# Kernel tuning notes

Measured on AMD Instinct MI355X. Metric: run time of the kernel, lower is better.

Reference implementation:

```python
import jax, jax.numpy as jnp
import numpy as np

B, T, H, NH = 2, 2048, 2048, 16
HD = H // NH  # 128


def setup_inputs() -> dict:
    key = jax.random.key(0)
    ks = jax.random.split(key, 7)
    s = 1.0 / np.sqrt(H)
    return {
        "x": jax.random.normal(ks[0], (B, T, H), jnp.float32),
        "cos": jax.random.uniform(ks[1], (1, 1, T, HD), jnp.float32),
        "sin": jax.random.uniform(ks[2], (1, 1, T, HD), jnp.float32),
        "Wq": jax.random.normal(ks[3], (H, H), jnp.float32) * s,
        "Wk": jax.random.normal(ks[4], (H, H), jnp.float32) * s,
        "Wv": jax.random.normal(ks[5], (H, H), jnp.float32) * s,
        "Wo": jax.random.normal(ks[6], (H, H), jnp.float32) * s,
    }


def rotate_half(x):
    d = x.shape[-1] // 2
    return jnp.concatenate([-x[..., d:], x[..., :d]], axis=-1)


def reference(x, cos, sin, Wq, Wk, Wv, Wo):
    b, t, h = x.shape
    # torch Linear: y = x @ W.T; reshape to (B, NH, T, HD)
    def proj(W):
        return jnp.einsum('bth,oh->bto', x, W).reshape(b, t, NH, HD).transpose(0, 2, 1, 3)
    q, k, v = proj(Wq), proj(Wk), proj(Wv)
    q = q * cos + rotate_half(q) * sin
    k = k * cos + rotate_half(k) * sin
    scale = 1.0 / jnp.sqrt(jnp.asarray(HD, x.dtype))
    scores = jnp.einsum('bhqd,bhkd->bhqk', q, k) * scale  # [B,NH,T,T]
    causal = jnp.tril(jnp.ones((t, t), bool))
    scores = jnp.where(causal, scores, jnp.asarray(-jnp.inf, scores.dtype))
    attn = jax.nn.softmax(scores, axis=-1)
    out = jnp.einsum('bhqk,bhkd->bhqd', attn, v)  # [B,NH,T,HD]
    out = out.transpose(0, 2, 1, 3).reshape(b, t, h)
    return jnp.einsum('bth,oh->bto', out, Wo)
```

## Files before the change

### kernel.cpp

```cpp
#include <hip/hip_runtime.h>
#include <hip/hip_bf16.h>

#define B_  2
#define T_  2048
#define H_  2048
#define NH_ 16
#define HD_ 128
#define QKVN 6144

typedef __attribute__((ext_vector_type(8))) short  short8;
typedef __attribute__((ext_vector_type(4))) float  floatx4;

__device__ __forceinline__ unsigned short f2bf(float x) {
    union { float f; unsigned int u; } c; c.f = x;
    unsigned int r = c.u + 0x7FFF + ((c.u >> 16) & 1);
    return (unsigned short)(r >> 16);
}
__device__ __forceinline__ float bf2f(unsigned short u) {
    union { float f; unsigned int i; } c;
    c.i = ((unsigned int)u) << 16;
    return c.f;
}

__device__ __forceinline__ void gload_lds16(const void* g, void* l) {
    __builtin_amdgcn_global_load_lds(
        (__attribute__((address_space(1))) void*)g,
        (__attribute__((address_space(3))) void*)l, 16, 0, 0);
}

__global__ __launch_bounds__(256) void f32_to_bf16(
    const float* __restrict__ src, unsigned short* __restrict__ dst, int n)
{
    const int i = (blockIdx.x * 256 + threadIdx.x) * 4;
    if (i < n) {
        float4 v = *(const float4*)(src + i);
        ushort4 o;
        o.x = f2bf(v.x); o.y = f2bf(v.y); o.z = f2bf(v.z); o.w = f2bf(v.w);
        *(ushort4*)(dst + i) = o;
    }
}

#define BAR()   asm volatile("s_barrier" ::: "memory")
#define SBAR()  __builtin_amdgcn_sched_barrier(0)
#define LGKM0() do { asm volatile("s_waitcnt lgkmcnt(0)" ::: "memory"); SBAR(); } while (0)
#define VM0()   asm volatile("s_waitcnt vmcnt(0)" ::: "memory")

template<int MI, int BASE>
__device__ __forceinline__ void ldAf(short8 (&d)[MI/2][2], const unsigned short* src,
                                     int wm, int n16, int quad)
{
    #pragma unroll
    for (int mi = 0; mi < MI/2; ++mi)
        #pragma unroll
        for (int ks = 0; ks < 2; ++ks)
            d[mi][ks] = *(const short8*)(src + (wm*(MI*16) + (BASE+mi)*16 + n16) * 64
                                             + (((ks*4 + quad) ^ (n16 & 7)) * 8));
}
template<int NI, int BASE>
__device__ __forceinline__ void ldBf(short8 (&d)[NI/2][2], const unsigned short* src,
                                     int wn, int n16, int quad)
{
    #pragma unroll
    for (int ni = 0; ni < NI/2; ++ni)
        #pragma unroll
        for (int ks = 0; ks < 2; ++ks)
            d[ni][ks] = *(const short8*)(src + (wn*(NI*16) + (BASE+ni)*16 + n16) * 64
                                             + (((ks*4 + quad) ^ (n16 & 7)) * 8));
}
template<int MI, int NI, int MB, int NB>
__device__ __forceinline__ void mq(floatx4 (&acc)[MI][NI],
                                   const short8 (&a)[MI/2][2],
                                   const short8 (&b)[NI/2][2])
{
    #pragma unroll
    for (int ks = 0; ks < 2; ++ks)
        #pragma unroll
        for (int mi = 0; mi < MI/2; ++mi)
            #pragma unroll
            for (int ni = 0; ni < NI/2; ++ni)
                acc[MB+mi][NB+ni] = __builtin_amdgcn_mfma_f32_16x16x32_bf16(
                    a[mi][ks], b[ni][ks], acc[MB+mi][NB+ni], 0, 0, 0);
}

template<int MI, int NI>
__device__ __forceinline__ void gt_tile(
    const unsigned short* Ac, const unsigned short* Bc,
    unsigned short* An, unsigned short* Bn,
    const unsigned short* Ap, const unsigned short* Bp,
    size_t knext, bool pre, int tid, int K,
    int wm, int wn, int n16, int quad,
    floatx4 (&acc)[MI][NI])
{
    constexpr int MH = MI/2, NH = NI/2;
    constexpr int AG = (MI*32)/64;
    constexpr int BG = (NI*64)/64;

    short8 aL[MH][2], aH[MH][2], bL[NH][2], bH[NH][2];

    ldAf<MI, 0>(aL, Ac, wm, n16, quad);
    ldBf<NI, 0>(bL, Bc, wn, n16, quad);
    if (pre) {
        #pragma unroll
        for (int h = 0; h < AG; ++h)
            gload_lds16(Ap + knext + (size_t)h * 64 * K, An + h * 4096 + (size_t)tid * 8);
    }
    BAR();
    LGKM0();
    __builtin_amdgcn_s_setprio(1);
    mq<MI, NI, 0, 0>(acc, aL, bL);
    __builtin_amdgcn_s_setprio(0);
    BAR();

    ldBf<NI, NH>(bH, Bc, wn, n16, quad);
    if (pre) {
        #pragma unroll
        for (int h = 0; h < BG; ++h)
            gload_lds16(Bp + knext + (size_t)h * 64 * K, Bn + h * 4096 + (size_t)tid * 8);
    }
    BAR();
    LGKM0();
    __builtin_amdgcn_s_setprio(1);
    mq<MI, NI, 0, NH>(acc, aL, bH);
    __builtin_amdgcn_s_setprio(0);
    BAR();

    ldAf<MI, MH>(aH, Ac, wm, n16, quad);
    BAR();
    LGKM0();
    __builtin_amdgcn_s_setprio(1);
    mq<MI, NI, MH, 0>(acc, aH, bL);
    __builtin_amdgcn_s_setprio(0);
    BAR();

    VM0();
    BAR();
    SBAR();
    __builtin_amdgcn_s_setprio(1);
    mq<MI, NI, MH, NH>(acc, aH, bH);
    __builtin_amdgcn_s_setprio(0);
    BAR();
}

template<int MI, int NI, bool BF16_OUT>
__global__ __launch_bounds__(512, 1) void gemm_t(
    const unsigned short* __restrict__ A,
    const unsigned short* __restrict__ W,
    float* __restrict__ Yf, unsigned short* __restrict__ Yb,
    int M, int N, int K)
{
    constexpr int BM = MI*32, BN = NI*64;
    constexpr int AG = BM/64, BG = BN/64;
    __shared__ __attribute__((aligned(16))) unsigned short As[2][BM * 64];
    __shared__ __attribute__((aligned(16))) unsigned short Bs[2][BN * 64];

    const int tid  = threadIdx.x;
    const int lane = tid & 63;
    const int n16  = lane & 15;
    const int quad = lane >> 4;
    const int w    = tid >> 6;
    const int wm   = w >> 2;
    const int wn   = w & 3;

    const int m0 = blockIdx.y * BM;
    const int n0 = blockIdx.x * BN;

    const int r0  = tid >> 3;
    const int g0  = ((tid & 7) ^ (r0 & 7)) * 8;
    const unsigned short* Ap = A + (size_t)(m0 + r0) * K + g0;
    const unsigned short* Bp = W + (size_t)(n0 + r0) * K + g0;

    floatx4 acc[MI][NI];
    #pragma unroll
    for (int i = 0; i < MI; i++)
        #pragma unroll
        for (int j = 0; j < NI; j++) acc[i][j] = (floatx4){0.f, 0.f, 0.f, 0.f};

    const int nt = K >> 6;

    #pragma unroll
    for (int h = 0; h < AG; ++h)
        gload_lds16(Ap + (size_t)h * 64 * K, &As[0][h * 4096 + (size_t)tid * 8]);
    #pragma unroll
    for (int h = 0; h < BG; ++h)
        gload_lds16(Bp + (size_t)h * 64 * K, &Bs[0][h * 4096 + (size_t)tid * 8]);
    VM0();
    BAR();

    for (int t = 0; t < nt; t += 2) {
        gt_tile<MI, NI>(&As[0][0], &Bs[0][0], &As[1][0], &Bs[1][0],
                        Ap, Bp, (size_t)(t + 1) << 6, (t + 1) < nt,
                        tid, K, wm, wn, n16, quad, acc);
        gt_tile<MI, NI>(&As[1][0], &Bs[1][0], &As[0][0], &Bs[0][0],
                        Ap, Bp, (size_t)(t + 2) << 6, (t + 2) < nt,
                        tid, K, wm, wn, n16, quad, acc);
    }

    #pragma unroll
    for (int mi = 0; mi < MI; ++mi) {
        const size_t rb = (size_t)(m0 + wm*(MI*16) + mi*16 + quad*4);
        #pragma unroll
        for (int r = 0; r < 4; ++r) {
            const size_t row = rb + r;
            #pragma unroll
            for (int ni = 0; ni < NI; ++ni) {
                const size_t col = n0 + wn*(NI*16) + ni*16 + n16;
                if (BF16_OUT) Yb[row * N + col] = f2bf(acc[mi][ni][r]);
                else          Yf[row * N + col] = acc[mi][ni][r];
            }
        }
    }
}

__global__ __launch_bounds__(256) void rope_convert_qk(
    const unsigned short* __restrict__ qkvp,
    const float* __restrict__ cosp, const float* __restrict__ sinp,
    unsigned short* __restrict__ qh, unsigned short* __restrict__ kh)
{
    const int idx  = blockIdx.x * 256 + threadIdx.x;
    const int d    = idx & 63;
    const int rest = idx >> 6;
    const int h    = rest & 15;
    const int bt   = rest >> 4;
    const int t    = bt & (T_ - 1);
    const int b    = bt >> 11;
    const size_t ibase = (size_t)bt * QKVN + h * HD_;
    const size_t obase = (((size_t)b * NH_ + h) * T_ + t) * HD_;

    const float c0 = cosp[t*HD_ + d],      s0 = sinp[t*HD_ + d];
    const float c1 = cosp[t*HD_ + d + 64], s1 = sinp[t*HD_ + d + 64];
    const float sc = 0.08838834764831845f;

    float q0 = bf2f(qkvp[ibase + d]), q1 = bf2f(qkvp[ibase + d + 64]);
    qh[obase + d]      = f2bf((q0*c0 - q1*s0) * sc);
    qh[obase + d + 64] = f2bf((q1*c1 + q0*s1) * sc);

    float k0 = bf2f(qkvp[ibase + 2048 + d]), k1 = bf2f(qkvp[ibase + 2048 + d + 64]);
    kh[obase + d]      = f2bf(k0*c0 - k1*s0);
    kh[obase + d + 64] = f2bf(k1*c1 + k0*s1);
}

__global__ __launch_bounds__(256) void transpose_v(
    const unsigned short* __restrict__ qkvp, unsigned short* __restrict__ vh)
{
    __shared__ float tile[64][65];
    const int t0 = blockIdx.x * 64;
    const int d0 = blockIdx.y * 64;
    const int bh = blockIdx.z;
    const int b  = bh >> 4, h = bh & 15;

    for (int i = threadIdx.x; i < 4096; i += 256) {
        int r = i >> 6, c = i & 63;
        tile[r][c] = bf2f(qkvp[((size_t)b*T_ + t0 + r) * QKVN + 4096 + h*HD_ + d0 + c]);
    }
    __syncthreads();
    for (int i = threadIdx.x; i < 4096; i += 256) {
        int dr = i >> 6, tc = i & 63;
        vh[((size_t)bh * HD_ + d0 + dr) * T_ + t0 + tc] = f2bf(tile[tc][dr]);
    }
}

__global__ __launch_bounds__(256, 4) void attn_mfma(
    const unsigned short* __restrict__ qh,
    const unsigned short* __restrict__ kh,
    const unsigned short* __restrict__ vh,
    unsigned short* __restrict__ o)
{
    __shared__ __attribute__((aligned(16))) unsigned short Ks[64 * 128];
    __shared__ __attribute__((aligned(16))) unsigned short Vs[128 * 64];
    __shared__ __attribute__((aligned(16))) unsigned short Ps[4][16 * 64];

    const int tid  = threadIdx.x;
    const int lane = tid & 63;
    const int w    = tid >> 6;
    const int n16  = lane & 15;
    const int quad = lane >> 4;

    const int id   = blockIdx.y * gridDim.x + blockIdx.x;
    const int bh   = id & 31;
    const int a    = (id >> 5) & 7;
    const int u    = id >> 8;
    const int qblk = (u < 2) ? (a + (u << 3)) : ((23 + ((u & 1) << 3)) - a);

    const int q0w  = qblk * 64 + w * 16;

    short8 qf[4];
    {
        const size_t qbase = ((size_t)bh * T_ + q0w + n16) * HD_ + quad * 8;
        #pragma unroll
        for (int c = 0; c < 4; c++)
            qf[c] = *(const short8*)(qh + qbase + c * 32);
    }

    const int rk   = tid >> 4;
    const int gk16 = ((tid & 15) ^ (rk & 7)) * 8;
    const unsigned short* ksrc = kh + (size_t)bh * T_ * HD_ + (size_t)rk * HD_ + gk16;
    const int dv   = tid >> 3;
    const int gv16 = ((tid & 7) ^ (dv & 7)) * 8;
    const unsigned short* vsrc = vh + (size_t)bh * HD_ * T_ + (size_t)dv * T_ + gv16;

    floatx4 of[8];
    #pragma unroll
    for (int i = 0; i < 8; i++) of[i] = (floatx4){0.f, 0.f, 0.f, 0.f};
    float mrow[4], lrow[4];
    #pragma unroll
    for (int r = 0; r < 4; r++) { mrow[r] = -INFINITY; lrow[r] = 0.f; }

    const int nkv = qblk + 1;
    for (int kv = 0; kv < nkv; kv++) {
        const int kv0 = kv * 64;
        __syncthreads();
        #pragma unroll
        for (int it = 0; it < 4; it++)
            gload_lds16(ksrc + (size_t)(kv0 + it * 16) * HD_,
                        Ks + (size_t)(it * 256 + tid) * 8);
        #pragma unroll
        for (int it = 0; it < 4; it++)
            gload_lds16(vsrc + kv0 + (size_t)(it * 32) * T_,
                        Vs + (size_t)(it * 256 + tid) * 8);
        __syncthreads();

        floatx4 s[4];
        #pragma unroll
        for (int kg = 0; kg < 4; kg++) {
            floatx4 acc = {0.f, 0.f, 0.f, 0.f};
            #pragma unroll
            for (int c = 0; c < 4; c++) {
                short8 kf = *(const short8*)(Ks + (kg*16 + n16) * 128
                                                + (((c*4 + quad) ^ (n16 & 7)) * 8));
                acc = __builtin_amdgcn_mfma_f32_16x16x32_bf16(qf[c], kf, acc, 0, 0, 0);
            }
            s[kg] = acc;
        }

        const bool needmask = (kv0 + 63 > q0w);

        float alpha[4];
        #pragma unroll
        for (int r = 0; r < 4; r++) {
            const int qrow = q0w + quad * 4 + r;
            float v0 = s[0][r], v1 = s[1][r], v2 = s[2][r], v3 = s[3][r];
            if (needmask) {
                if (kv0 +  0 + n16 > qrow) v0 = -INFINITY;
                if (kv0 + 16 + n16 > qrow) v1 = -INFINITY;
                if (kv0 + 32 + n16 > qrow) v2 = -INFINITY;
                if (kv0 + 48 + n16 > qrow) v3 = -INFINITY;
            }

            float tm = fmaxf(fmaxf(v0, v1), fmaxf(v2, v3));
            tm = fmaxf(tm, __shfl_xor(tm, 1));
            tm = fmaxf(tm, __shfl_xor(tm, 2));
            tm = fmaxf(tm, __shfl_xor(tm, 4));
            tm = fmaxf(tm, __shfl_xor(tm, 8));

            const float mnew = fmaxf(mrow[r], tm);
            const float aa   = __expf(mrow[r] - mnew);
            const float p0 = __expf(v0 - mnew), p1 = __expf(v1 - mnew);
            const float p2 = __expf(v2 - mnew), p3 = __expf(v3 - mnew);

            float ts = p0 + p1 + p2 + p3;
            ts += __shfl_xor(ts, 1);
            ts += __shfl_xor(ts, 2);
            ts += __shfl_xor(ts, 4);
            ts += __shfl_xor(ts, 8);

            lrow[r] = lrow[r] * aa + ts;
            mrow[r] = mnew;
            alpha[r] = aa;

            const int pr = quad * 4 + r;
            const int sx = pr & 7;
            unsigned short* pp = &Ps[w][pr * 64];
            const int g0p = n16 >> 3, e = n16 & 7;
            pp[((g0p    ) ^ sx) * 8 + e] = f2bf(p0);
            pp[((g0p + 2) ^ sx) * 8 + e] = f2bf(p1);
            pp[((g0p + 4) ^ sx) * 8 + e] = f2bf(p2);
            pp[((g0p + 6) ^ sx) * 8 + e] = f2bf(p3);
        }
        #pragma unroll
        for (int nt = 0; nt < 8; nt++)
            #pragma unroll
            for (int r = 0; r < 4; r++) of[nt][r] *= alpha[r];

        short8 pf0 = *(const short8*)(&Ps[w][n16 * 64 + ((quad       ^ (n16 & 7)) * 8)]);
        short8 pf1 = *(const short8*)(&Ps[w][n16 * 64 + (((quad + 4) ^ (n16 & 7)) * 8)]);
        #pragma unroll
        for (int nt = 0; nt < 8; nt++) {
            const int vr = (nt * 16 + n16) * 64;
            short8 vf0 = *(const short8*)(Vs + vr + ((quad       ^ (n16 & 7)) * 8));
            short8 vf1 = *(const short8*)(Vs + vr + (((quad + 4) ^ (n16 & 7)) * 8));
            of[nt] = __builtin_amdgcn_mfma_f32_16x16x32_bf16(pf0, vf0, of[nt], 0, 0, 0);
            of[nt] = __builtin_amdgcn_mfma_f32_16x16x32_bf16(pf1, vf1, of[nt], 0, 0, 0);
        }
    }

    const int b = bh >> 4, h = bh & 15;
    #pragma unroll
    for (int r = 0; r < 4; r++) {
        const float inv = 1.f / lrow[r];
        const size_t orow = ((size_t)b * T_ + q0w + quad*4 + r) * H_ + h * HD_;
        #pragma unroll
        for (int nt = 0; nt < 8; nt++)
            o[orow + nt*16 + n16] = f2bf(of[nt][r] * inv);
    }
}

extern "C" void kernel_launch(void* const* d_in, const int* in_sizes, int n_in,
                              void* d_out, int out_size, void* d_ws, size_t ws_size,
                              hipStream_t stream)
{
    const float* x    = (const float*)d_in[0];
    const float* cosp = (const float*)d_in[1];
    const float* sinp = (const float*)d_in[2];
    const float* Wq   = (const float*)d_in[3];
    const float* Wk   = (const float*)d_in[4];
    const float* Wv   = (const float*)d_in[5];
    const float* Wo   = (const float*)d_in[6];

    const size_t NEL  = (size_t)B_ * T_ * H_;
    const int    XN   = (int)NEL;
    const int    WN   = H_ * H_;
    char* ws = (char*)d_ws;
    const size_t MB16 = 16777216;

    unsigned short* xh    = (unsigned short*)(ws);
    unsigned short* Wqkvh = (unsigned short*)(ws + MB16);
    unsigned short* Woh   = (unsigned short*)(ws + MB16*5/2);
    unsigned short* qkvp  = (unsigned short*)(ws + 3*MB16);
    unsigned short* kh    = (unsigned short*)(ws + 6*MB16);
    unsigned short* qh    = (unsigned short*)(ws + MB16);
    unsigned short* vh    = (unsigned short*)(ws);
    unsigned short* abh   = (unsigned short*)(ws + 3*MB16);

    f32_to_bf16<<<XN/1024, 256, 0, stream>>>(x,  xh,  XN);
    f32_to_bf16<<<WN/1024, 256, 0, stream>>>(Wq, Wqkvh,          WN);
    f32_to_bf16<<<WN/1024, 256, 0, stream>>>(Wk, Wqkvh +   WN,   WN);
    f32_to_bf16<<<WN/1024, 256, 0, stream>>>(Wv, Wqkvh + 2*WN,   WN);
    f32_to_bf16<<<WN/1024, 256, 0, stream>>>(Wo, Woh,            WN);

    const int M = B_ * T_;

    gemm_t<4, 6, true><<<dim3(QKVN/384, M/128), 512, 0, stream>>>(
        xh, Wqkvh, nullptr, qkvp, M, QKVN, H_);

    rope_convert_qk<<<(B_*T_*NH_*64)/256, 256, 0, stream>>>(qkvp, cosp, sinp, qh, kh);
    transpose_v<<<dim3(T_/64, HD_/64, B_*NH_), 256, 0, stream>>>(qkvp, vh);

    attn_mfma<<<dim3(T_/64, B_*NH_), 256, 0, stream>>>(qh, kh, vh, abh);

    gemm_t<4, 4, false><<<dim3(H_/256, M/128), 512, 0, stream>>>(
        abh, Woh, (float*)d_out, nullptr, M, H_, H_);
}
```

Baseline: 430.5 us.

## Triple-buffer GEMM LDS tiles and prefetch two stages ahead with one barrier

The GEMM main loop moves from a double-buffered scheme, with four barrier/waitcnt phases per K-tile and interleaved LDS reads and MFMA chunks, to a triple-buffered ring. Global-to-LDS loads for tile t+2 are issued at the start of each tile, all fragments are read from LDS, all MFMAs run, and a partial vmcnt(6) wait plus a single barrier closes the tile. The aim is to cut per-tile synchronization and hide more global-load latency. The QKV projection also drops from a 4x6 to a 4x4 wave tile so the triple buffer fits in LDS and the fixed vmcnt count matches. Costs are larger LDS use, the loss of the finer MFMA/LDS-read interleaving and s_setprio hints, and smaller QKV tiles with less reuse.

```diff
diff --git a/kernel.cpp b/kernel.cpp
--- a/kernel.cpp
+++ b/kernel.cpp
@@ -41,9 +41,6 @@
 }
 
 #define BAR()   asm volatile("s_barrier" ::: "memory")
-#define SBAR()  __builtin_amdgcn_sched_barrier(0)
-#define LGKM0() do { asm volatile("s_waitcnt lgkmcnt(0)" ::: "memory"); SBAR(); } while (0)
-#define VM0()   asm volatile("s_waitcnt vmcnt(0)" ::: "memory")
 
 template<int MI, int BASE>
 __device__ __forceinline__ void ldAf(short8 (&d)[MI/2][2], const unsigned short* src,
@@ -85,7 +82,7 @@
 template<int MI, int NI>
 __device__ __forceinline__ void gt_tile(
     const unsigned short* Ac, const unsigned short* Bc,
-    unsigned short* An, unsigned short* Bn,
+    unsigned short* An2, unsigned short* Bn2,
     const unsigned short* Ap, const unsigned short* Bp,
     size_t knext, bool pre, int tid, int K,
     int wm, int wn, int n16, int quad,
@@ -95,49 +92,28 @@
     constexpr int AG = (MI*32)/64;
     constexpr int BG = (NI*64)/64;
 
+    if (pre) {
+        #pragma unroll
+        for (int h = 0; h < AG; ++h)
+            gload_lds16(Ap + knext + (size_t)h * 64 * K, An2 + h * 4096 + (size_t)tid * 8);
+        #pragma unroll
+        for (int h = 0; h < BG; ++h)
+            gload_lds16(Bp + knext + (size_t)h * 64 * K, Bn2 + h * 4096 + (size_t)tid * 8);
+    }
+
     short8 aL[MH][2], aH[MH][2], bL[NH][2], bH[NH][2];
-
-    ldAf<MI, 0>(aL, Ac, wm, n16, quad);
-    ldBf<NI, 0>(bL, Bc, wn, n16, quad);
-    if (pre) {
-        #pragma unroll
-        for (int h = 0; h < AG; ++h)
-            gload_lds16(Ap + knext + (size_t)h * 64 * K, An + h * 4096 + (size_t)tid * 8);
-    }
-    BAR();
-    LGKM0();
-    __builtin_amdgcn_s_setprio(1);
-    mq<MI, NI, 0, 0>(acc, aL, bL);
-    __builtin_amdgcn_s_setprio(0);
-    BAR();
-
+    ldAf<MI, 0 >(aL, Ac, wm, n16, quad);
+    ldBf<NI, 0 >(bL, Bc, wn, n16, quad);
+    ldAf<MI, MH>(aH, Ac, wm, n16, quad);
     ldBf<NI, NH>(bH, Bc, wn, n16, quad);
-    if (pre) {
-        #pragma unroll
-        for (int h = 0; h < BG; ++h)
-            gload_lds16(Bp + knext + (size_t)h * 64 * K, Bn + h * 4096 + (size_t)tid * 8);
-    }
-    BAR();
-    LGKM0();
-    __builtin_amdgcn_s_setprio(1);
-    mq<MI, NI, 0, NH>(acc, aL, bH);
-    __builtin_amdgcn_s_setprio(0);
-    BAR();
-
-    ldAf<MI, MH>(aH, Ac, wm, n16, quad);
-    BAR();
-    LGKM0();
-    __builtin_amdgcn_s_setprio(1);
-    mq<MI, NI, MH, 0>(acc, aH, bL);
-    __builtin_amdgcn_s_setprio(0);
-    BAR();
-
-    VM0();
-    BAR();
-    SBAR();
-    __builtin_amdgcn_s_setprio(1);
+
+    mq<MI, NI, 0,  0 >(acc, aL, bL);
+    mq<MI, NI, 0,  NH>(acc, aL, bH);
+    mq<MI, NI, MH, 0 >(acc, aH, bL);
     mq<MI, NI, MH, NH>(acc, aH, bH);
-    __builtin_amdgcn_s_setprio(0);
+
+    if (pre) asm volatile("s_waitcnt vmcnt(6)" ::: "memory");
+    else     asm volatile("s_waitcnt vmcnt(0)" ::: "memory");
     BAR();
 }
 
@@ -150,8 +126,8 @@
 {
     constexpr int BM = MI*32, BN = NI*64;
     constexpr int AG = BM/64, BG = BN/64;
-    __shared__ __attribute__((aligned(16))) unsigned short As[2][BM * 64];
-    __shared__ __attribute__((aligned(16))) unsigned short Bs[2][BN * 64];
+    __shared__ __attribute__((aligned(16))) unsigned short As[3][BM * 64];
+    __shared__ __attribute__((aligned(16))) unsigned short Bs[3][BN * 64];
 
     const int tid  = threadIdx.x;
     const int lane = tid & 63;
@@ -183,16 +159,24 @@
     #pragma unroll
     for (int h = 0; h < BG; ++h)
         gload_lds16(Bp + (size_t)h * 64 * K, &Bs[0][h * 4096 + (size_t)tid * 8]);
-    VM0();
+    #pragma unroll
+    for (int h = 0; h < AG; ++h)
+        gload_lds16(Ap + 64 + (size_t)h * 64 * K, &As[1][h * 4096 + (size_t)tid * 8]);
+    #pragma unroll
+    for (int h = 0; h < BG; ++h)
+        gload_lds16(Bp + 64 + (size_t)h * 64 * K, &Bs[1][h * 4096 + (size_t)tid * 8]);
+    asm volatile("s_waitcnt vmcnt(6)" ::: "memory");
     BAR();
 
-    for (int t = 0; t < nt; t += 2) {
-        gt_tile<MI, NI>(&As[0][0], &Bs[0][0], &As[1][0], &Bs[1][0],
-                        Ap, Bp, (size_t)(t + 1) << 6, (t + 1) < nt,
-                        tid, K, wm, wn, n16, quad, acc);
-        gt_tile<MI, NI>(&As[1][0], &Bs[1][0], &As[0][0], &Bs[0][0],
+    const unsigned short *a0 = &As[0][0], *a1 = &As[1][0], *a2 = &As[2][0];
+    const unsigned short *b0 = &Bs[0][0], *b1 = &Bs[1][0], *b2 = &Bs[2][0];
+
+    for (int t = 0; t < nt; ++t) {
+        gt_tile<MI, NI>(a0, b0, (unsigned short*)a2, (unsigned short*)b2,
                         Ap, Bp, (size_t)(t + 2) << 6, (t + 2) < nt,
                         tid, K, wm, wn, n16, quad, acc);
+        const unsigned short* ta = a0; a0 = a1; a1 = a2; a2 = ta;
+        const unsigned short* tb = b0; b0 = b1; b1 = b2; b2 = tb;
     }
 
     #pragma unroll
@@ -439,7 +423,7 @@
 
     const int M = B_ * T_;
 
-    gemm_t<4, 6, true><<<dim3(QKVN/384, M/128), 512, 0, stream>>>(
+    gemm_t<4, 4, true><<<dim3(QKVN/256, M/128), 512, 0, stream>>>(
         xh, Wqkvh, nullptr, qkvp, M, QKVN, H_);
 
     rope_convert_qk<<<(B_*T_*NH_*64)/256, 256, 0, stream>>>(qkvp, cosp, sinp, qh, kh);
```

Measured after the change: 446.9 us. +3.8%, slower.
